# Kernel optimization log

Measured on AMD Instinct MI355X. Metric: run time of the kernel, lower is better.

The kernel has to match this reference:

```python
import jax, jax.numpy as jnp
import numpy as np

B, L, E, H, D, OUT = 4, 2048, 1024, 8, 128, 1024


def setup_inputs() -> dict:
    key = jax.random.key(0)
    ks = jax.random.split(key, 6)
    stdv = 1.0 / np.sqrt(D)
    return {
        "k": jax.random.normal(ks[0], (B, L, E), dtype=jnp.float32),
        "q": jax.random.normal(ks[1], (B, L, E), dtype=jnp.float32),
        "w_kx": jax.random.uniform(ks[2], (H, E, D), minval=-stdv, maxval=stdv, dtype=jnp.float32),
        "w_qx": jax.random.uniform(ks[3], (H, E, D), minval=-stdv, maxval=stdv, dtype=jnp.float32),
        "proj_w": jax.random.normal(ks[4], (OUT, H * D), dtype=jnp.float32) * 0.02,
        "proj_b": jnp.zeros((OUT,), dtype=jnp.float32),
        "flag": False,
    }


def reference(k, q, w_kx, w_qx, proj_w, proj_b, flag):
    # Per-head sigmoid projections, vectorized over heads (original loops over heads).
    d = w_kx.shape[-1]
    kx = jax.nn.sigmoid(jnp.einsum('ble,hed->bhld', k, w_kx))  # [B,H,Lk,D]
    if flag:
        # flag==True: q is used directly (already hidden_dim-sized), shared across heads
        qx = jnp.broadcast_to(q[:, None], (q.shape[0], kx.shape[1], q.shape[1], q.shape[2]))
    else:
        qx = jax.nn.sigmoid(jnp.einsum('bqe,hed->bhqd', q, w_qx))  # [B,H,Lq,D]
    # scaled dot-product score + softmax over key axis
    score = jnp.einsum('bhqd,bhkd->bhqk', qx, kx) * (1.0 / jnp.sqrt(jnp.asarray(d, kx.dtype)))
    attn = jax.nn.softmax(score, axis=-1)
    out = jnp.einsum('bhqk,bhkd->bhqd', attn, kx)  # [B,H,Lq,D]
    # concat heads along feature dim, then linear projection (dropout p=0 -> identity)
    b, h, lq, _ = out.shape
    out = out.transpose(0, 2, 1, 3).reshape(b, lq, h * d)
    return out @ proj_w.T + proj_b
```

## Files before the change

### kernel.cpp

```cpp
#include <hip/hip_runtime.h>

#define BB 4
#define LL 2048
#define EE 1024
#define HH 8
#define DD 128
#define OO 1024
#define MM (BB*LL)
#define ND (HH*DD)

#define QBLK 128
#define KVBLK 64
#define NT (LL / KVBLK)

#define C2 0.12751920678739807f

typedef __bf16 bf16;
typedef unsigned short u16;
typedef __bf16 bf16x8 __attribute__((ext_vector_type(8)));
typedef __bf16 bf16x4 __attribute__((ext_vector_type(4)));
typedef float  f32x4  __attribute__((ext_vector_type(4)));

__device__ __forceinline__ void gl16(const bf16* g, bf16* l) {
#if __has_builtin(__builtin_amdgcn_global_load_lds)
    __builtin_amdgcn_global_load_lds((const __attribute__((address_space(1))) char*)g,
                                     (__attribute__((address_space(3))) char*)l, 16, 0, 0);
#else
    *(bf16x8*)l = *(const bf16x8*)g;
#endif
}

__device__ __forceinline__ bf16x8 cvt8(const float* s) {
    float4 f0 = *(const float4*)s;
    float4 f1 = *(const float4*)(s + 4);
    bf16x8 v;
    v[0] = (bf16)f0.x; v[1] = (bf16)f0.y; v[2] = (bf16)f0.z; v[3] = (bf16)f0.w;
    v[4] = (bf16)f1.x; v[5] = (bf16)f1.y; v[6] = (bf16)f1.z; v[7] = (bf16)f1.w;
    return v;
}

__global__ void detect_kernel(const u16* __restrict__ data, int* __restrict__ mode) {
    const int l = threadIdx.x;
    int cnt = 0;
#pragma unroll
    for (int i = 0; i < 8; i++) {
        int e = (data[l * 8 + i] >> 7) & 0xFF;
        cnt += (e >= 117 && e <= 132) ? 1 : 0;
    }
    cnt += __shfl_xor(cnt, 1);
    cnt += __shfl_xor(cnt, 2);
    cnt += __shfl_xor(cnt, 4);
    cnt += __shfl_xor(cnt, 8);
    cnt += __shfl_xor(cnt, 16);
    cnt += __shfl_xor(cnt, 32);
    if (l == 0) *mode = (cnt > 400) ? 1 : 0;
}

__global__ __launch_bounds__(256) void fill_kernel(float* __restrict__ out, float v, int n) {
    int i = blockIdx.x * 256 + threadIdx.x;
    if (i < n) out[i] = v;
}

__global__ __launch_bounds__(256) void wtrans_kernel(const void* __restrict__ in0,
                                                     const void* __restrict__ in1,
                                                     bf16* __restrict__ outT0,
                                                     bf16* __restrict__ outT1,
                                                     const int* __restrict__ mode) {
    const void* in = blockIdx.y ? in1 : in0;
    bf16* outT = blockIdx.y ? outT1 : outT0;
    int idx = blockIdx.x * 256 + threadIdx.x;
    int i4 = idx * 4;
    int h = i4 >> 17;
    int rem = i4 & 131071;
    int e = rem >> 7;
    int d = rem & 127;
    size_t ob = ((size_t)h * DD + d) * EE + e;
    if (*mode) {
        bf16x4 v = *(const bf16x4*)((const bf16*)in + i4);
        outT[ob]          = v[0];
        outT[ob + EE]     = v[1];
        outT[ob + 2 * EE] = v[2];
        outT[ob + 3 * EE] = v[3];
    } else {
        float4 v = *(const float4*)((const float*)in + i4);
        outT[ob]          = (bf16)v.x;
        outT[ob + EE]     = (bf16)v.y;
        outT[ob + 2 * EE] = (bf16)v.z;
        outT[ob + 3 * EE] = (bf16)v.w;
    }
}

__global__ __launch_bounds__(256) void gemm_kernel(const void* __restrict__ A0,
                                                   const void* __restrict__ A1,
                                                   const void* __restrict__ BT0,
                                                   const void* __restrict__ BT1,
                                                   bf16* __restrict__ outBF0,
                                                   bf16* __restrict__ outBF1,
                                                   bf16* __restrict__ outT,
                                                   float* __restrict__ outF,
                                                   const void* __restrict__ PB,
                                                   const int* __restrict__ mode,
                                                   const int epi) {
    __shared__ __align__(16) bf16 As[128 * 64];
    __shared__ __align__(16) bf16 Bs[128 * 64];
    const int md = *mode;
    const int aBf = (epi == 2) ? 1 : md;
    const int bBf = (epi == 2) ? md : 1;
    const int t = threadIdx.x;
    const int w = t >> 6, l = t & 63;
    const int lr = l & 15, lg = l >> 4;
    const int wr = w >> 1, wc = w & 1;
    const int o = blockIdx.x + (blockIdx.y << 3);
    const int half = (epi == 3) ? (o >> 9) : 0;
    const int oo = o & 511;
    const int mt = (oo & 7) * 8 + ((oo >> 3) & 7);
    const int ntile = oo >> 6;
    const int m0 = mt * 128, n0 = ntile * 128;
    const void* A = half ? A1 : A0;
    const void* BT = half ? BT1 : BT0;

    f32x4 acc[4][4];
    const f32x4 zero = {0.f, 0.f, 0.f, 0.f};
#pragma unroll
    for (int i = 0; i < 4; i++)
#pragma unroll
        for (int j = 0; j < 4; j++) acc[i][j] = zero;

    for (int kt = 0; kt < 16; ++kt) {
        const int k0 = kt * 64;
        __syncthreads();
        if (aBf) {
#pragma unroll
            for (int p = 0; p < 4; p++) {
                const int id = p * 256 + t;
                const int row = id >> 3;
                const int c = (id & 7) ^ (row & 7);
                gl16((const bf16*)A + (size_t)(m0 + row) * 1024 + k0 + c * 8,
                     As + (p * 256 + w * 64) * 8);
            }
        } else {
#pragma unroll
            for (int p = 0; p < 4; p++) {
                const int id = p * 256 + t;
                const int row = id >> 3;
                const int cc = id & 7;
                bf16x8 v = cvt8((const float*)A + (size_t)(m0 + row) * 1024 + k0 + cc * 8);
                *(bf16x8*)(As + row * 64 + ((cc ^ (row & 7)) << 3)) = v;
            }
        }
        if (bBf) {
#pragma unroll
            for (int p = 0; p < 4; p++) {
                const int id = p * 256 + t;
                const int row = id >> 3;
                const int c = (id & 7) ^ (row & 7);
                gl16((const bf16*)BT + (size_t)(n0 + row) * 1024 + k0 + c * 8,
                     Bs + (p * 256 + w * 64) * 8);
            }
        } else {
#pragma unroll
            for (int p = 0; p < 4; p++) {
                const int id = p * 256 + t;
                const int row = id >> 3;
                const int cc = id & 7;
                bf16x8 v = cvt8((const float*)BT + (size_t)(n0 + row) * 1024 + k0 + cc * 8);
                *(bf16x8*)(Bs + row * 64 + ((cc ^ (row & 7)) << 3)) = v;
            }
        }
        __syncthreads();
        bf16x8 af[4][2], bg[4][2];
#pragma unroll
        for (int i = 0; i < 4; i++) {
            const int ar = wr * 64 + i * 16 + lr;
#pragma unroll
            for (int ks = 0; ks < 2; ks++)
                af[i][ks] = *(const bf16x8*)(As + ar * 64 + (((ks * 4 + lg) ^ (ar & 7)) << 3));
        }
#pragma unroll
        for (int j = 0; j < 4; j++) {
            const int br = wc * 64 + j * 16 + lr;
#pragma unroll
            for (int ks = 0; ks < 2; ks++)
                bg[j][ks] = *(const bf16x8*)(Bs + br * 64 + (((ks * 4 + lg) ^ (br & 7)) << 3));
        }
#pragma unroll
        for (int i = 0; i < 4; i++)
#pragma unroll
            for (int j = 0; j < 4; j++) {
                acc[i][j] = __builtin_amdgcn_mfma_f32_16x16x32_bf16(af[i][0], bg[j][0], acc[i][j], 0, 0, 0);
                acc[i][j] = __builtin_amdgcn_mfma_f32_16x16x32_bf16(af[i][1], bg[j][1], acc[i][j], 0, 0, 0);
            }
    }

    if (epi == 3) {
        bf16* outBF = half ? outBF1 : outBF0;
        const float mulf = half ? C2 : 1.0f;
        const int b_idx = m0 >> 11;
        const int h = n0 >> 7;
#pragma unroll
        for (int i = 0; i < 4; i++) {
#pragma unroll
            for (int j = 0; j < 4; j++) {
                const int gr = m0 + wr * 64 + i * 16 + lg * 4;
                const int gc = n0 + wc * 64 + j * 16 + lr;
                float s0 = mulf / (1.0f + __expf(-acc[i][j][0]));
                float s1 = mulf / (1.0f + __expf(-acc[i][j][1]));
                float s2 = mulf / (1.0f + __expf(-acc[i][j][2]));
                float s3 = mulf / (1.0f + __expf(-acc[i][j][3]));
                outBF[(size_t)gr * ND + gc]           = (bf16)s0;
                outBF[(size_t)(gr + 1) * ND + gc]     = (bf16)s1;
                outBF[(size_t)(gr + 2) * ND + gc]     = (bf16)s2;
                outBF[(size_t)(gr + 3) * ND + gc]     = (bf16)s3;
                if (!half) {
                    bf16x4 pk;
                    pk[0] = (bf16)s0; pk[1] = (bf16)s1; pk[2] = (bf16)s2; pk[3] = (bf16)s3;
                    const int d = gc & 127;
                    const int lrow = gr & 2047;
                    *(bf16x4*)(outT + (((size_t)(h * BB + b_idx)) * DD + d) * LL + lrow) = pk;
                }
            }
        }
    } else {
#pragma unroll
        for (int j = 0; j < 4; j++) {
            const int gc = n0 + wc * 64 + j * 16 + lr;
            const float bias = md ? (float)((const bf16*)PB)[gc] : ((const float*)PB)[gc];
#pragma unroll
            for (int i = 0; i < 4; i++) {
                const int gr = m0 + wr * 64 + i * 16 + lg * 4;
#pragma unroll
                for (int reg = 0; reg < 4; reg++)
                    outF[(size_t)(gr + reg) * OO + gc] = acc[i][j][reg] + bias;
            }
        }
    }
}

__global__ __launch_bounds__(512, 4) void attn_kernel(const bf16* __restrict__ QX,
                                                      const bf16* __restrict__ KX,
                                                      const bf16* __restrict__ KXT,
                                                      bf16* __restrict__ AO) {
    __shared__ __align__(16) bf16 Kl[2][KVBLK * 128];
    __shared__ __align__(16) bf16 Vt[2][128 * KVBLK];
    __shared__ __align__(16) bf16 Pl[8][16 * 64];
    const int t = threadIdx.x;
    const int w = t >> 6, l = t & 63;
    const int lr = l & 15, lg = l >> 4;
    const int bid = blockIdx.x;
    const int orig = (bid & 7) * 64 + (bid >> 3);
    const int bh = orig >> 4;
    const int h = bh & 7, b = bh >> 3;
    const int q0 = (orig & 15) * QBLK;
    const bf16* qxh = QX + (size_t)(b * LL) * ND + h * DD;
    const bf16* kxh = KX + (size_t)(b * LL) * ND + h * DD;
    const bf16* kxt = KXT + ((size_t)(h * BB + b)) * DD * LL;

    const int kid1 = 512 + t;
    const int krow0 = t >> 4,    kcc0 = t & 15;
    const int krow1 = kid1 >> 4, kcc1 = kid1 & 15;
    const int vrow0 = t >> 3,    vcc0 = t & 7;
    const int vrow1 = kid1 >> 3, vcc1 = kid1 & 7;
    const bf16* kp0 = kxh + (size_t)krow0 * ND + kcc0 * 8;
    const bf16* kp1 = kxh + (size_t)krow1 * ND + kcc1 * 8;
    const bf16* vp0 = kxt + (size_t)vrow0 * LL + vcc0 * 8;
    const bf16* vp1 = kxt + (size_t)vrow1 * LL + vcc1 * 8;
    const int kw0 = krow0 * 128 + ((kcc0 ^ (krow0 & 15)) << 3);
    const int kw1 = krow1 * 128 + ((kcc1 ^ (krow1 & 15)) << 3);
    const int vw0 = vrow0 * 64 + ((vcc0 ^ (vrow0 & 7)) << 3);
    const int vw1 = vrow1 * 64 + ((vcc1 ^ (vrow1 & 7)) << 3);

    bf16x8 qf[4];
    const int qrow = q0 + w * 16 + lr;
#pragma unroll
    for (int s = 0; s < 4; s++)
        qf[s] = *(const bf16x8*)(qxh + (size_t)qrow * ND + s * 32 + lg * 8);

    bf16x8 rk0 = *(const bf16x8*)(kp0);
    bf16x8 rk1 = *(const bf16x8*)(kp1);
    bf16x8 rv0 = *(const bf16x8*)(vp0);
    bf16x8 rv1 = *(const bf16x8*)(vp1);
    *(bf16x8*)(Kl[0] + kw0) = rk0;
    *(bf16x8*)(Kl[0] + kw1) = rk1;
    *(bf16x8*)(Vt[0] + vw0) = rv0;
    *(bf16x8*)(Vt[0] + vw1) = rv1;
    rk0 = *(const bf16x8*)(kp0 + (size_t)KVBLK * ND);
    rk1 = *(const bf16x8*)(kp1 + (size_t)KVBLK * ND);
    rv0 = *(const bf16x8*)(vp0 + KVBLK);
    rv1 = *(const bf16x8*)(vp1 + KVBLK);
    __syncthreads();

    f32x4 oacc[8];
    const f32x4 zero = {0.f, 0.f, 0.f, 0.f};
#pragma unroll
    for (int n = 0; n < 8; n++) oacc[n] = zero;
    float psum = 0.f;

    for (int kt = 0; kt < NT; ++kt) {
        const int cur = kt & 1;
        if (kt + 1 < NT) {
            *(bf16x8*)(Kl[cur ^ 1] + kw0) = rk0;
            *(bf16x8*)(Kl[cur ^ 1] + kw1) = rk1;
            *(bf16x8*)(Vt[cur ^ 1] + vw0) = rv0;
            *(bf16x8*)(Vt[cur ^ 1] + vw1) = rv1;
            if (kt + 2 < NT) {
                const size_t ko = (size_t)(kt + 2) * KVBLK * ND;
                const int vo = (kt + 2) * KVBLK;
                rk0 = *(const bf16x8*)(kp0 + ko);
                rk1 = *(const bf16x8*)(kp1 + ko);
                rv0 = *(const bf16x8*)(vp0 + vo);
                rv1 = *(const bf16x8*)(vp1 + vo);
            }
        }
        const bf16* KlC = Kl[cur];
        const bf16* VtC = Vt[cur];

        f32x4 sa[4];
        __builtin_amdgcn_s_setprio(1);
#pragma unroll
        for (int n = 0; n < 4; n++) {
            sa[n] = zero;
#pragma unroll
            for (int ks = 0; ks < 4; ks++) {
                int arow = n * 16 + lr;
                bf16x8 kb = *(const bf16x8*)(KlC + arow * 128 + ((((ks * 4 + lg) ^ (arow & 15))) << 3));
                sa[n] = __builtin_amdgcn_mfma_f32_16x16x32_bf16(kb, qf[ks], sa[n], 0, 0, 0);
            }
        }
        __builtin_amdgcn_s_setprio(0);
#pragma unroll
        for (int n = 0; n < 4; n++) {
            bf16x4 pk;
#pragma unroll
            for (int j = 0; j < 4; j++) {
                float p = exp2f(sa[n][j]);
                psum += p;
                pk[j] = (bf16)p;
            }
            const int chunk = (2 * n + (lg >> 1)) ^ (lr & 7);
            *(bf16x4*)(Pl[w] + lr * 64 + chunk * 8 + (lg & 1) * 4) = pk;
        }
        asm volatile("s_waitcnt lgkmcnt(0)" ::: "memory");
        __builtin_amdgcn_sched_barrier(0);
        bf16x8 pb0 = *(const bf16x8*)(Pl[w] + lr * 64 + (((lg ^ (lr & 7))) << 3));
        bf16x8 pb1 = *(const bf16x8*)(Pl[w] + lr * 64 + ((((4 + lg) ^ (lr & 7))) << 3));
        __builtin_amdgcn_s_setprio(1);
#pragma unroll
        for (int n = 0; n < 8; n++) {
            int vrow = n * 16 + lr;
            bf16x8 vb0 = *(const bf16x8*)(VtC + vrow * 64 + (((lg ^ (vrow & 7))) << 3));
            oacc[n] = __builtin_amdgcn_mfma_f32_16x16x32_bf16(vb0, pb0, oacc[n], 0, 0, 0);
            bf16x8 vb1 = *(const bf16x8*)(VtC + vrow * 64 + ((((4 + lg) ^ (vrow & 7))) << 3));
            oacc[n] = __builtin_amdgcn_mfma_f32_16x16x32_bf16(vb1, pb1, oacc[n], 0, 0, 0);
        }
        __builtin_amdgcn_s_setprio(0);
        __syncthreads();
    }
    float tot = psum;
    tot += __shfl_xor(tot, 16);
    tot += __shfl_xor(tot, 32);
    const float linv = 1.0f / tot;
    const int arow = b * LL + q0 + w * 16 + lr;
    bf16* aoRow = AO + (size_t)arow * ND + h * DD;
#pragma unroll
    for (int n = 0; n < 8; n++) {
        bf16x4 o;
#pragma unroll
        for (int reg = 0; reg < 4; reg++) o[reg] = (bf16)(oacc[n][reg] * linv);
        *(bf16x4*)(aoRow + n * 16 + lg * 4) = o;
    }
}

extern "C" void kernel_launch(void* const* d_in, const int* in_sizes, int n_in,
                              void* d_out, int out_size, void* d_ws, size_t ws_size,
                              hipStream_t stream) {
    (void)in_sizes; (void)n_in;
    float* out = (float*)d_out;

    const size_t NEED = ((size_t)(2 + 2 + 16 + 16 + 16 + 16) << 20) + 256;
    if (ws_size < NEED) {
        hipLaunchKernelGGL(fill_kernel, dim3((out_size + 255) / 256), dim3(256), 0, stream,
                           out, (float)(ws_size >> 20), out_size);
        return;
    }

    int* mode = (int*)d_ws;
    bf16* base = (bf16*)((char*)d_ws + 256);
    bf16* wkT = base;
    bf16* wqT = wkT + (size_t)HH * DD * EE;
    bf16* kx  = wqT + (size_t)HH * DD * EE;
    bf16* qx  = kx  + (size_t)MM * ND;
    bf16* kxT = qx  + (size_t)MM * ND;
    bf16* ao  = kxT + (size_t)HH * MM * DD;

    hipLaunchKernelGGL(detect_kernel, dim3(1), dim3(64), 0, stream, (const u16*)d_in[0], mode);
    hipLaunchKernelGGL(wtrans_kernel, dim3(HH * EE * DD / 4 / 256, 2), dim3(256), 0, stream,
                       d_in[2], d_in[3], wkT, wqT, mode);
    hipLaunchKernelGGL(gemm_kernel, dim3(8, 128), dim3(256), 0, stream,
                       d_in[0], d_in[1], wkT, wqT, kx, qx, kxT,
                       (float*)nullptr, (const void*)nullptr, mode, 3);
    hipLaunchKernelGGL(attn_kernel, dim3(512), dim3(512), 0, stream, qx, kx, kxT, ao);
    hipLaunchKernelGGL(gemm_kernel, dim3(8, 64), dim3(256), 0, stream,
                       ao, (const void*)nullptr, d_in[4], (const void*)nullptr,
                       (bf16*)nullptr, (bf16*)nullptr, (bf16*)nullptr, out, d_in[5], mode, 2);
}
```

Baseline: 195.0 us.

## Stage transposed K output through LDS and unroll attention loop by two

The GEMM epilogue for the K projection now writes the transposed copy into a padded shared-memory tile and then emits coalesced 16-byte row stores, replacing scattered 8-byte strided global writes. The attention loop is unrolled by two with compile-time buffer indices and precomputed LDS pointers, removing per-iteration address arithmetic. This adds two barriers and a larger shared allocation in the GEMM kernel, which may lower occupancy.

```diff
diff --git a/kernel.cpp b/kernel.cpp
--- a/kernel.cpp
+++ b/kernel.cpp
@@ -101,8 +101,9 @@
                                                    const void* __restrict__ PB,
                                                    const int* __restrict__ mode,
                                                    const int epi) {
-    __shared__ __align__(16) bf16 As[128 * 64];
-    __shared__ __align__(16) bf16 Bs[128 * 64];
+    __shared__ __align__(16) char smem[34816];
+    bf16* As = (bf16*)smem;
+    bf16* Bs = (bf16*)(smem + 16384);
     const int md = *mode;
     const int aBf = (epi == 2) ? 1 : md;
     const int bBf = (epi == 2) ? md : 1;
@@ -195,28 +196,55 @@
     if (epi == 3) {
         bf16* outBF = half ? outBF1 : outBF0;
         const float mulf = half ? C2 : 1.0f;
-        const int b_idx = m0 >> 11;
-        const int h = n0 >> 7;
-#pragma unroll
-        for (int i = 0; i < 4; i++) {
-#pragma unroll
-            for (int j = 0; j < 4; j++) {
-                const int gr = m0 + wr * 64 + i * 16 + lg * 4;
-                const int gc = n0 + wc * 64 + j * 16 + lr;
-                float s0 = mulf / (1.0f + __expf(-acc[i][j][0]));
-                float s1 = mulf / (1.0f + __expf(-acc[i][j][1]));
-                float s2 = mulf / (1.0f + __expf(-acc[i][j][2]));
-                float s3 = mulf / (1.0f + __expf(-acc[i][j][3]));
-                outBF[(size_t)gr * ND + gc]           = (bf16)s0;
-                outBF[(size_t)(gr + 1) * ND + gc]     = (bf16)s1;
-                outBF[(size_t)(gr + 2) * ND + gc]     = (bf16)s2;
-                outBF[(size_t)(gr + 3) * ND + gc]     = (bf16)s3;
-                if (!half) {
+        if (!half) {
+            bf16* sT = (bf16*)smem;
+            __syncthreads();
+#pragma unroll
+            for (int i = 0; i < 4; i++) {
+#pragma unroll
+                for (int j = 0; j < 4; j++) {
+                    const int gr = m0 + wr * 64 + i * 16 + lg * 4;
+                    const int gc = n0 + wc * 64 + j * 16 + lr;
+                    const int d = gc & 127;
+                    const int mloc = wr * 64 + i * 16 + lg * 4;
+                    float s0 = mulf / (1.0f + __expf(-acc[i][j][0]));
+                    float s1 = mulf / (1.0f + __expf(-acc[i][j][1]));
+                    float s2 = mulf / (1.0f + __expf(-acc[i][j][2]));
+                    float s3 = mulf / (1.0f + __expf(-acc[i][j][3]));
+                    outBF[(size_t)gr * ND + gc]       = (bf16)s0;
+                    outBF[(size_t)(gr + 1) * ND + gc] = (bf16)s1;
+                    outBF[(size_t)(gr + 2) * ND + gc] = (bf16)s2;
+                    outBF[(size_t)(gr + 3) * ND + gc] = (bf16)s3;
                     bf16x4 pk;
                     pk[0] = (bf16)s0; pk[1] = (bf16)s1; pk[2] = (bf16)s2; pk[3] = (bf16)s3;
-                    const int d = gc & 127;
-                    const int lrow = gr & 2047;
-                    *(bf16x4*)(outT + (((size_t)(h * BB + b_idx)) * DD + d) * LL + lrow) = pk;
+                    *(bf16x4*)(sT + d * 136 + mloc) = pk;
+                }
+            }
+            __syncthreads();
+            const int b_idx = m0 >> 11;
+            const int h = n0 >> 7;
+            const int lrow0 = m0 & 2047;
+            const int d = t >> 1, mh = (t & 1) * 64;
+            const bf16* srcRow = sT + d * 136 + mh;
+            bf16* dstRow = outT + (((size_t)(h * BB + b_idx)) * DD + d) * LL + lrow0 + mh;
+#pragma unroll
+            for (int c = 0; c < 8; c++)
+                *(bf16x8*)(dstRow + c * 8) = *(const bf16x8*)(srcRow + c * 8);
+        } else {
+#pragma unroll
+            for (int i = 0; i < 4; i++) {
+#pragma unroll
+                for (int j = 0; j < 4; j++) {
+                    const int gr = m0 + wr * 64 + i * 16 + lg * 4;
+                    const int gc = n0 + wc * 64 + j * 16 + lr;
+                    float s0 = mulf / (1.0f + __expf(-acc[i][j][0]));
+                    float s1 = mulf / (1.0f + __expf(-acc[i][j][1]));
+                    float s2 = mulf / (1.0f + __expf(-acc[i][j][2]));
+                    float s3 = mulf / (1.0f + __expf(-acc[i][j][3]));
+                    outBF[(size_t)gr * ND + gc]       = (bf16)s0;
+                    outBF[(size_t)(gr + 1) * ND + gc] = (bf16)s1;
+                    outBF[(size_t)(gr + 2) * ND + gc] = (bf16)s2;
+                    outBF[(size_t)(gr + 3) * ND + gc] = (bf16)s3;
                 }
             }
         }
@@ -240,8 +268,8 @@
                                                       const bf16* __restrict__ KX,
                                                       const bf16* __restrict__ KXT,
                                                       bf16* __restrict__ AO) {
-    __shared__ __align__(16) bf16 Kl[2][KVBLK * 128];
-    __shared__ __align__(16) bf16 Vt[2][128 * KVBLK];
+    __shared__ __align__(16) bf16 Kl[2 * KVBLK * 128];
+    __shared__ __align__(16) bf16 Vt[2 * 128 * KVBLK];
     __shared__ __align__(16) bf16 Pl[8][16 * 64];
     const int t = threadIdx.x;
     const int w = t >> 6, l = t & 63;
@@ -260,14 +288,31 @@
     const int krow1 = kid1 >> 4, kcc1 = kid1 & 15;
     const int vrow0 = t >> 3,    vcc0 = t & 7;
     const int vrow1 = kid1 >> 3, vcc1 = kid1 & 7;
-    const bf16* kp0 = kxh + (size_t)krow0 * ND + kcc0 * 8;
-    const bf16* kp1 = kxh + (size_t)krow1 * ND + kcc1 * 8;
-    const bf16* vp0 = kxt + (size_t)vrow0 * LL + vcc0 * 8;
-    const bf16* vp1 = kxt + (size_t)vrow1 * LL + vcc1 * 8;
-    const int kw0 = krow0 * 128 + ((kcc0 ^ (krow0 & 15)) << 3);
-    const int kw1 = krow1 * 128 + ((kcc1 ^ (krow1 & 15)) << 3);
-    const int vw0 = vrow0 * 64 + ((vcc0 ^ (vrow0 & 7)) << 3);
-    const int vw1 = vrow1 * 64 + ((vcc1 ^ (vrow1 & 7)) << 3);
+    const bf16* kpr0 = kxh + (size_t)krow0 * ND + kcc0 * 8;
+    const bf16* kpr1 = kxh + (size_t)krow1 * ND + kcc1 * 8;
+    const bf16* vpr0 = kxt + (size_t)vrow0 * LL + vcc0 * 8;
+    const bf16* vpr1 = kxt + (size_t)vrow1 * LL + vcc1 * 8;
+    bf16* kwp0 = Kl + krow0 * 128 + ((kcc0 ^ (krow0 & 15)) << 3);
+    bf16* kwp1 = Kl + krow1 * 128 + ((kcc1 ^ (krow1 & 15)) << 3);
+    bf16* vwp0 = Vt + vrow0 * 64 + ((vcc0 ^ (vrow0 & 7)) << 3);
+    bf16* vwp1 = Vt + vrow1 * 64 + ((vcc1 ^ (vrow1 & 7)) << 3);
+
+    const bf16* vK[4];
+#pragma unroll
+    for (int ks = 0; ks < 4; ks++)
+        vK[ks] = Kl + lr * 128 + (((ks * 4 + lg) ^ lr) << 3);
+    const bf16* vV[2];
+#pragma unroll
+    for (int x = 0; x < 2; x++)
+        vV[x] = Vt + lr * 64 + (((x * 4 + lg) ^ (lr & 7)) << 3);
+    bf16* pwp[4];
+#pragma unroll
+    for (int n = 0; n < 4; n++) {
+        const int chunk = (2 * n + (lg >> 1)) ^ (lr & 7);
+        pwp[n] = Pl[w] + lr * 64 + chunk * 8 + (lg & 1) * 4;
+    }
+    const bf16* prp0 = Pl[w] + lr * 64 + ((lg ^ (lr & 7)) << 3);
+    const bf16* prp1 = Pl[w] + lr * 64 + (((4 + lg) ^ (lr & 7)) << 3);
 
     bf16x8 qf[4];
     const int qrow = q0 + w * 16 + lr;
@@ -275,18 +320,16 @@
     for (int s = 0; s < 4; s++)
         qf[s] = *(const bf16x8*)(qxh + (size_t)qrow * ND + s * 32 + lg * 8);
 
-    bf16x8 rk0 = *(const bf16x8*)(kp0);
-    bf16x8 rk1 = *(const bf16x8*)(kp1);
-    bf16x8 rv0 = *(const bf16x8*)(vp0);
-    bf16x8 rv1 = *(const bf16x8*)(vp1);
-    *(bf16x8*)(Kl[0] + kw0) = rk0;
-    *(bf16x8*)(Kl[0] + kw1) = rk1;
-    *(bf16x8*)(Vt[0] + vw0) = rv0;
-    *(bf16x8*)(Vt[0] + vw1) = rv1;
-    rk0 = *(const bf16x8*)(kp0 + (size_t)KVBLK * ND);
-    rk1 = *(const bf16x8*)(kp1 + (size_t)KVBLK * ND);
-    rv0 = *(const bf16x8*)(vp0 + KVBLK);
-    rv1 = *(const bf16x8*)(vp1 + KVBLK);
+    bf16x8 rk0 = *(const bf16x8*)kpr0;
+    bf16x8 rk1 = *(const bf16x8*)kpr1;
+    bf16x8 rv0 = *(const bf16x8*)vpr0;
+    bf16x8 rv1 = *(const bf16x8*)vpr1;
+    *(bf16x8*)kwp0 = rk0;  *(bf16x8*)kwp1 = rk1;
+    *(bf16x8*)vwp0 = rv0;  *(bf16x8*)vwp1 = rv1;
+    kpr0 += (size_t)KVBLK * ND;  kpr1 += (size_t)KVBLK * ND;
+    vpr0 += KVBLK;               vpr1 += KVBLK;
+    rk0 = *(const bf16x8*)kpr0;  rk1 = *(const bf16x8*)kpr1;
+    rv0 = *(const bf16x8*)vpr0;  rv1 = *(const bf16x8*)vpr1;
     __syncthreads();
 
     f32x4 oacc[8];
@@ -295,66 +338,60 @@
     for (int n = 0; n < 8; n++) oacc[n] = zero;
     float psum = 0.f;
 
-    for (int kt = 0; kt < NT; ++kt) {
-        const int cur = kt & 1;
-        if (kt + 1 < NT) {
-            *(bf16x8*)(Kl[cur ^ 1] + kw0) = rk0;
-            *(bf16x8*)(Kl[cur ^ 1] + kw1) = rk1;
-            *(bf16x8*)(Vt[cur ^ 1] + vw0) = rv0;
-            *(bf16x8*)(Vt[cur ^ 1] + vw1) = rv1;
-            if (kt + 2 < NT) {
-                const size_t ko = (size_t)(kt + 2) * KVBLK * ND;
-                const int vo = (kt + 2) * KVBLK;
-                rk0 = *(const bf16x8*)(kp0 + ko);
-                rk1 = *(const bf16x8*)(kp1 + ko);
-                rv0 = *(const bf16x8*)(vp0 + vo);
-                rv1 = *(const bf16x8*)(vp1 + vo);
-            }
-        }
-        const bf16* KlC = Kl[cur];
-        const bf16* VtC = Vt[cur];
-
-        f32x4 sa[4];
-        __builtin_amdgcn_s_setprio(1);
-#pragma unroll
-        for (int n = 0; n < 4; n++) {
-            sa[n] = zero;
-#pragma unroll
-            for (int ks = 0; ks < 4; ks++) {
-                int arow = n * 16 + lr;
-                bf16x8 kb = *(const bf16x8*)(KlC + arow * 128 + ((((ks * 4 + lg) ^ (arow & 15))) << 3));
-                sa[n] = __builtin_amdgcn_mfma_f32_16x16x32_bf16(kb, qf[ks], sa[n], 0, 0, 0);
-            }
-        }
-        __builtin_amdgcn_s_setprio(0);
-#pragma unroll
-        for (int n = 0; n < 4; n++) {
-            bf16x4 pk;
-#pragma unroll
-            for (int j = 0; j < 4; j++) {
-                float p = exp2f(sa[n][j]);
-                psum += p;
-                pk[j] = (bf16)p;
-            }
-            const int chunk = (2 * n + (lg >> 1)) ^ (lr & 7);
-            *(bf16x4*)(Pl[w] + lr * 64 + chunk * 8 + (lg & 1) * 4) = pk;
-        }
-        asm volatile("s_waitcnt lgkmcnt(0)" ::: "memory");
-        __builtin_amdgcn_sched_barrier(0);
-        bf16x8 pb0 = *(const bf16x8*)(Pl[w] + lr * 64 + (((lg ^ (lr & 7))) << 3));
-        bf16x8 pb1 = *(const bf16x8*)(Pl[w] + lr * 64 + ((((4 + lg) ^ (lr & 7))) << 3));
-        __builtin_amdgcn_s_setprio(1);
-#pragma unroll
-        for (int n = 0; n < 8; n++) {
-            int vrow = n * 16 + lr;
-            bf16x8 vb0 = *(const bf16x8*)(VtC + vrow * 64 + (((lg ^ (vrow & 7))) << 3));
-            oacc[n] = __builtin_amdgcn_mfma_f32_16x16x32_bf16(vb0, pb0, oacc[n], 0, 0, 0);
-            bf16x8 vb1 = *(const bf16x8*)(VtC + vrow * 64 + ((((4 + lg) ^ (vrow & 7))) << 3));
-            oacc[n] = __builtin_amdgcn_mfma_f32_16x16x32_bf16(vb1, pb1, oacc[n], 0, 0, 0);
-        }
-        __builtin_amdgcn_s_setprio(0);
-        __syncthreads();
-    }
+#define ATTN_TILE(KT, CUR)                                                     \
+    {                                                                          \
+        if ((KT) + 1 < NT) {                                                   \
+            *(bf16x8*)(kwp0 + ((CUR) ^ 1) * 8192) = rk0;                       \
+            *(bf16x8*)(kwp1 + ((CUR) ^ 1) * 8192) = rk1;                       \
+            *(bf16x8*)(vwp0 + ((CUR) ^ 1) * 8192) = rv0;                       \
+            *(bf16x8*)(vwp1 + ((CUR) ^ 1) * 8192) = rv1;                       \
+            if ((KT) + 2 < NT) {                                               \
+                kpr0 += (size_t)KVBLK * ND;  kpr1 += (size_t)KVBLK * ND;       \
+                vpr0 += KVBLK;               vpr1 += KVBLK;                     \
+                rk0 = *(const bf16x8*)kpr0;  rk1 = *(const bf16x8*)kpr1;       \
+                rv0 = *(const bf16x8*)vpr0;  rv1 = *(const bf16x8*)vpr1;       \
+            }                                                                  \
+        }                                                                      \
+        f32x4 sa[4];                                                           \
+        __builtin_amdgcn_s_setprio(1);                                         \
+        _Pragma("unroll") for (int n = 0; n < 4; n++) {                        \
+            sa[n] = zero;                                                      \
+            _Pragma("unroll") for (int ks = 0; ks < 4; ks++) {                 \
+                bf16x8 kb = *(const bf16x8*)(vK[ks] + (CUR) * 8192 + n * 2048);\
+                sa[n] = __builtin_amdgcn_mfma_f32_16x16x32_bf16(kb, qf[ks], sa[n], 0, 0, 0); \
+            }                                                                  \
+        }                                                                      \
+        __builtin_amdgcn_s_setprio(0);                                         \
+        _Pragma("unroll") for (int n = 0; n < 4; n++) {                        \
+            bf16x4 pk;                                                         \
+            _Pragma("unroll") for (int j = 0; j < 4; j++) {                    \
+                float p = exp2f(sa[n][j]);                                     \
+                psum += p;                                                     \
+                pk[j] = (bf16)p;                                               \
+            }                                                                  \
+            *(bf16x4*)(pwp[n]) = pk;                                           \
+        }                                                                      \
+        asm volatile("s_waitcnt lgkmcnt(0)" ::: "memory");                     \
+        __builtin_amdgcn_sched_barrier(0);                                     \
+        bf16x8 pb0 = *(const bf16x8*)prp0;                                     \
+        bf16x8 pb1 = *(const bf16x8*)prp1;                                     \
+        __builtin_amdgcn_s_setprio(1);                                         \
+        _Pragma("unroll") for (int n = 0; n < 8; n++) {                        \
+            bf16x8 vb0 = *(const bf16x8*)(vV[0] + (CUR) * 8192 + n * 1024);    \
+            oacc[n] = __builtin_amdgcn_mfma_f32_16x16x32_bf16(vb0, pb0, oacc[n], 0, 0, 0); \
+            bf16x8 vb1 = *(const bf16x8*)(vV[1] + (CUR) * 8192 + n * 1024);    \
+            oacc[n] = __builtin_amdgcn_mfma_f32_16x16x32_bf16(vb1, pb1, oacc[n], 0, 0, 0); \
+        }                                                                      \
+        __builtin_amdgcn_s_setprio(0);                                         \
+        __syncthreads();                                                       \
+    }
+
+    for (int kt = 0; kt < NT; kt += 2) {
+        ATTN_TILE(kt, 0)
+        ATTN_TILE(kt + 1, 1)
+    }
+#undef ATTN_TILE
+
     float tot = psum;
     tot += __shfl_xor(tot, 16);
     tot += __shfl_xor(tot, 32);
```

Measured after the change: 200.0 us. 2.5% more time.
